# Performance work log

Measured on AMD Instinct MI355X. Metric: run time of the kernel, lower is better.

The kernel has to match this reference:

```python
import jax, jax.numpy as jnp
import numpy as np

LENGTH_SCALE = 0.1


def setup_inputs() -> dict:
    key = jax.random.key(0)
    k1, k2, k3 = jax.random.split(key, 3)
    features = jax.random.normal(k1, (8, 512, 128, 128), dtype=jnp.float32)
    # nn.Parameter init: normal(0, 0.05)
    weights = jax.random.normal(k2, (16, 64, 512), dtype=jnp.float32) * 0.05
    m = jax.random.normal(k3, (16, 64), dtype=jnp.float32)
    N = jnp.ones((64,), dtype=jnp.float32) * 12.0  # buffer init: ones * 12
    return {"features": features, "weights": weights, "m": m, "N": N}


def reference(features, weights, m, N):
    # per-class linear embedding projection: [b,f,h,w] x [e,c,f] -> [b,e,c,h,w]
    embeddings = jnp.einsum('bfhw,ecf->bechw', features, weights)
    centroids = m / N  # [e, c]
    gamma = -1.0 / (2.0 * LENGTH_SCALE ** 2)
    diff = embeddings - centroids[None, :, :, None, None]
    # squared L2, mean over embedding dim e, RBF exp -> [b, c, h, w]
    out = jnp.exp(jnp.mean(diff * diff, axis=1) * gamma)
    return out
```

## Files before the change

### kernel.cpp

```cpp
#include <hip/hip_runtime.h>

typedef __attribute__((ext_vector_type(8))) short bf16x8;
typedef __attribute__((ext_vector_type(4))) float f32x4;
typedef __attribute__((ext_vector_type(4))) float f4;
typedef __attribute__((ext_vector_type(2))) unsigned int u32x2;
typedef __attribute__((ext_vector_type(4))) unsigned int u32x4;

#define HW   16384
#define FDIM 512

__device__ __forceinline__ unsigned pkhi(float a, float b) {
    return __builtin_amdgcn_perm(__builtin_bit_cast(unsigned int, b),
                                 __builtin_bit_cast(unsigned int, a),
                                 0x07060302u);
}
__device__ __forceinline__ float trhi(float a) {
    return __builtin_bit_cast(float, __builtin_bit_cast(unsigned int, a) & 0xFFFF0000u);
}
__device__ __forceinline__ unsigned pklo(float a, float b) {
    return pkhi(a - trhi(a), b - trhi(b));
}

__global__ __launch_bounds__(256) void conv_w(const float* __restrict__ wts,
                                              unsigned short* __restrict__ wh,
                                              unsigned short* __restrict__ wl) {
    const int tid = blockIdx.x * 256 + threadIdx.x;
    const int n  = tid & 1023;
    const int kc = tid >> 10;
    const float* src = wts + (size_t)((n & 15) * 64 + (n >> 4)) * FDIM + kc * 8;
    f4 a = *(const f4*)src, b = *(const f4*)(src + 4);
    u32x4 h = { pkhi(a[0], a[1]), pkhi(a[2], a[3]), pkhi(b[0], b[1]), pkhi(b[2], b[3]) };
    u32x4 l = { pklo(a[0], a[1]), pklo(a[2], a[3]), pklo(b[0], b[1]), pklo(b[2], b[3]) };
    size_t off = ((size_t)kc * 1024 + n) * 8;
    *(u32x4*)(wh + off) = h;
    *(u32x4*)(wl + off) = l;
}

__global__ __launch_bounds__(256, 4) void duq_main(
    const float* __restrict__ feat,
    const unsigned short* __restrict__ wh,
    const unsigned short* __restrict__ wl,
    const float* __restrict__ m_in,
    const float* __restrict__ n_in,
    float* __restrict__ out)
{
    __shared__ __align__(16) unsigned short Ah[128 * 40];
    __shared__ __align__(16) unsigned short Al[128 * 40];

    const int t  = threadIdx.x;
    const int bx = blockIdx.x;
    const int kb = bx >> 3;
    const int nb = kb & 7;
    const int mb = (bx & 7) * 128 + (kb >> 3);
    const int bidx = mb >> 7;
    const int hw0  = (mb & 127) << 7;

    const int fb = t & 7;
    const int pb = t >> 3;
    const float* ap = feat + (size_t)bidx * (FDIM * HW) + (size_t)(fb * 4) * HW + (hw0 + pb * 4);
    unsigned short* awH = &Ah[(pb * 4) * 40 + fb * 4];
    unsigned short* awL = &Al[(pb * 4) * 40 + fb * 4];

    const int lane = t & 63;
    const int wv = t >> 6;
    const int wm = wv >> 1, wn = wv & 1;
    const int l16 = lane & 15, qd = lane >> 4;

    const unsigned short* arH = &Ah[(wm * 64 + l16) * 40 + qd * 8];
    const unsigned short* arL = &Al[(wm * 64 + l16) * 40 + qd * 8];

    const size_t bgoff = ((size_t)qd * 1024 + (size_t)(nb * 128 + wn * 64 + l16)) * 8;
    const unsigned short* bgh = wh + bgoff;
    const unsigned short* bgl = wl + bgoff;

    f32x4 acc[4][4] = {};

    f4 av[4];
    #pragma unroll
    for (int i = 0; i < 4; ++i) av[i] = *(const f4*)(ap + (size_t)i * HW);

    bf16x8 cbh = *(const bf16x8*)(bgh);
    bf16x8 cbl = *(const bf16x8*)(bgl);
    size_t boff = 0;

    for (int kt = 0; kt < 16; ++kt) {
        __syncthreads();
        #pragma unroll
        for (int j = 0; j < 4; ++j) {
            float a0 = av[0][j], a1 = av[1][j], a2 = av[2][j], a3 = av[3][j];
            u32x2 h, l;
            h[0] = pkhi(a0, a1); h[1] = pkhi(a2, a3);
            l[0] = pklo(a0, a1); l[1] = pklo(a2, a3);
            *(u32x2*)(awH + j * 40) = h;
            *(u32x2*)(awL + j * 40) = l;
        }
        __syncthreads();

        if (kt < 15) {
            ap += 32 * HW;
            #pragma unroll
            for (int i = 0; i < 4; ++i) av[i] = *(const f4*)(ap + (size_t)i * HW);
        }

        bf16x8 fah[4], fal[4];
        #pragma unroll
        for (int i = 0; i < 4; ++i) {
            fah[i] = *(const bf16x8*)(arH + i * 640);
            fal[i] = *(const bf16x8*)(arL + i * 640);
        }

        #pragma unroll
        for (int j = 0; j < 4; ++j) {
            size_t bnext = boff + ((j == 3) ? (size_t)(32768 - 384) : (size_t)128);
            bf16x8 nbh = *(const bf16x8*)(bgh + bnext);
            bf16x8 nbl = *(const bf16x8*)(bgl + bnext);
            #pragma unroll
            for (int i = 0; i < 4; ++i) {
                acc[i][j] = __builtin_amdgcn_mfma_f32_16x16x32_bf16(fah[i], cbh, acc[i][j], 0, 0, 0);
                acc[i][j] = __builtin_amdgcn_mfma_f32_16x16x32_bf16(fah[i], cbl, acc[i][j], 0, 0, 0);
                acc[i][j] = __builtin_amdgcn_mfma_f32_16x16x32_bf16(fal[i], cbh, acc[i][j], 0, 0, 0);
            }
            cbh = nbh; cbl = nbl; boff = bnext;
        }
    }

    float centv[4];
    #pragma unroll
    for (int j = 0; j < 4; ++j) {
        int cj = nb * 8 + wn * 4 + j;
        centv[j] = m_in[l16 * 64 + cj] / n_in[cj];
    }
    #pragma unroll
    for (int i = 0; i < 4; ++i) {
        #pragma unroll
        for (int j = 0; j < 4; ++j) {
            float s0 = acc[i][j][0] - centv[j]; s0 *= s0;
            float s1 = acc[i][j][1] - centv[j]; s1 *= s1;
            float s2 = acc[i][j][2] - centv[j]; s2 *= s2;
            float s3 = acc[i][j][3] - centv[j]; s3 *= s3;
            #pragma unroll
            for (int msk = 1; msk < 16; msk <<= 1) {
                s0 += __shfl_xor(s0, msk, 64);
                s1 += __shfl_xor(s1, msk, 64);
                s2 += __shfl_xor(s2, msk, 64);
                s3 += __shfl_xor(s3, msk, 64);
            }
            if (l16 == 0) {
                int cj = nb * 8 + wn * 4 + j;
                f4 o;
                o[0] = __expf(s0 * -3.125f);
                o[1] = __expf(s1 * -3.125f);
                o[2] = __expf(s2 * -3.125f);
                o[3] = __expf(s3 * -3.125f);
                size_t off = ((size_t)(bidx * 64 + cj)) * HW
                           + (size_t)(hw0 + wm * 64 + i * 16 + qd * 4);
                *(f4*)(out + off) = o;
            }
        }
    }
}

__global__ __launch_bounds__(256) void duq_fallback(
    const float* __restrict__ feat, const float* __restrict__ wts,
    const float* __restrict__ m_in, const float* __restrict__ n_in,
    float* __restrict__ out)
{
    __shared__ __align__(16) unsigned short Ah[128 * 40];
    __shared__ __align__(16) unsigned short Al[128 * 40];
    __shared__ __align__(16) unsigned short Bh[128 * 40];
    __shared__ __align__(16) unsigned short Bl[128 * 40];

    const int t  = threadIdx.x;
    const int bx = blockIdx.x;
    const int nb = bx & 7;
    const int mb = bx >> 3;
    const int bidx = mb >> 7;
    const int hw0  = (mb & 127) << 7;

    const int fb = t & 7;
    const int pb = t >> 3;
    const float* ap = feat + (size_t)bidx * (FDIM * HW) + (size_t)(fb * 4) * HW + (hw0 + pb * 4);

    const int bn  = t >> 1;
    const int bh_ = t & 1;
    const int ng  = nb * 128 + bn;
    const float* bp = wts + (size_t)((ng & 15) * 64 + (ng >> 4)) * FDIM + bh_ * 16;

    unsigned short* awH = &Ah[(pb * 4) * 40 + fb * 4];
    unsigned short* awL = &Al[(pb * 4) * 40 + fb * 4];
    unsigned short* bwH = &Bh[bn * 40 + bh_ * 16];
    unsigned short* bwL = &Bl[bn * 40 + bh_ * 16];

    const int lane = t & 63;
    const int wv = t >> 6;
    const int wm = wv >> 1, wn = wv & 1;
    const int l16 = lane & 15, qd = lane >> 4;

    const unsigned short* arH = &Ah[(wm * 64 + l16) * 40 + qd * 8];
    const unsigned short* arL = &Al[(wm * 64 + l16) * 40 + qd * 8];
    const unsigned short* brH = &Bh[(wn * 64 + l16) * 40 + qd * 8];
    const unsigned short* brL = &Bl[(wn * 64 + l16) * 40 + qd * 8];

    f32x4 acc[4][4] = {};

    f4 av[4], bv[4];
    #pragma unroll
    for (int i = 0; i < 4; ++i) av[i] = *(const f4*)(ap + (size_t)i * HW);
    #pragma unroll
    for (int q = 0; q < 4; ++q) bv[q] = *(const f4*)(bp + q * 4);

    for (int kt = 0; kt < 16; ++kt) {
        __syncthreads();
        #pragma unroll
        for (int j = 0; j < 4; ++j) {
            float a0 = av[0][j], a1 = av[1][j], a2 = av[2][j], a3 = av[3][j];
            u32x2 h, l;
            h[0] = pkhi(a0, a1); h[1] = pkhi(a2, a3);
            l[0] = pklo(a0, a1); l[1] = pklo(a2, a3);
            *(u32x2*)(awH + j * 40) = h;
            *(u32x2*)(awL + j * 40) = l;
        }
        {
            u32x4 h0 = { pkhi(bv[0][0], bv[0][1]), pkhi(bv[0][2], bv[0][3]),
                         pkhi(bv[1][0], bv[1][1]), pkhi(bv[1][2], bv[1][3]) };
            u32x4 h1 = { pkhi(bv[2][0], bv[2][1]), pkhi(bv[2][2], bv[2][3]),
                         pkhi(bv[3][0], bv[3][1]), pkhi(bv[3][2], bv[3][3]) };
            u32x4 l0 = { pklo(bv[0][0], bv[0][1]), pklo(bv[0][2], bv[0][3]),
                         pklo(bv[1][0], bv[1][1]), pklo(bv[1][2], bv[1][3]) };
            u32x4 l1 = { pklo(bv[2][0], bv[2][1]), pklo(bv[2][2], bv[2][3]),
                         pklo(bv[3][0], bv[3][1]), pklo(bv[3][2], bv[3][3]) };
            *(u32x4*)(bwH)     = h0;  *(u32x4*)(bwH + 8) = h1;
            *(u32x4*)(bwL)     = l0;  *(u32x4*)(bwL + 8) = l1;
        }
        __syncthreads();

        if (kt < 15) {
            ap += 32 * HW;
            bp += 32;
            #pragma unroll
            for (int i = 0; i < 4; ++i) av[i] = *(const f4*)(ap + (size_t)i * HW);
            #pragma unroll
            for (int q = 0; q < 4; ++q) bv[q] = *(const f4*)(bp + q * 4);
        }

        bf16x8 fah[4], fal[4];
        #pragma unroll
        for (int i = 0; i < 4; ++i) {
            fah[i] = *(const bf16x8*)(arH + i * 640);
            fal[i] = *(const bf16x8*)(arL + i * 640);
        }
        #pragma unroll
        for (int j = 0; j < 4; ++j) {
            bf16x8 fbh = *(const bf16x8*)(brH + j * 640);
            bf16x8 fbl = *(const bf16x8*)(brL + j * 640);
            #pragma unroll
            for (int i = 0; i < 4; ++i) {
                acc[i][j] = __builtin_amdgcn_mfma_f32_16x16x32_bf16(fah[i], fbh, acc[i][j], 0, 0, 0);
                acc[i][j] = __builtin_amdgcn_mfma_f32_16x16x32_bf16(fah[i], fbl, acc[i][j], 0, 0, 0);
                acc[i][j] = __builtin_amdgcn_mfma_f32_16x16x32_bf16(fal[i], fbh, acc[i][j], 0, 0, 0);
            }
        }
    }

    float centv[4];
    #pragma unroll
    for (int j = 0; j < 4; ++j) {
        int cj = nb * 8 + wn * 4 + j;
        centv[j] = m_in[l16 * 64 + cj] / n_in[cj];
    }
    #pragma unroll
    for (int i = 0; i < 4; ++i) {
        #pragma unroll
        for (int j = 0; j < 4; ++j) {
            float s0 = acc[i][j][0] - centv[j]; s0 *= s0;
            float s1 = acc[i][j][1] - centv[j]; s1 *= s1;
            float s2 = acc[i][j][2] - centv[j]; s2 *= s2;
            float s3 = acc[i][j][3] - centv[j]; s3 *= s3;
            #pragma unroll
            for (int msk = 1; msk < 16; msk <<= 1) {
                s0 += __shfl_xor(s0, msk, 64);
                s1 += __shfl_xor(s1, msk, 64);
                s2 += __shfl_xor(s2, msk, 64);
                s3 += __shfl_xor(s3, msk, 64);
            }
            if (l16 == 0) {
                int cj = nb * 8 + wn * 4 + j;
                f4 o;
                o[0] = __expf(s0 * -3.125f);
                o[1] = __expf(s1 * -3.125f);
                o[2] = __expf(s2 * -3.125f);
                o[3] = __expf(s3 * -3.125f);
                size_t off = ((size_t)(bidx * 64 + cj)) * HW
                           + (size_t)(hw0 + wm * 64 + i * 16 + qd * 4);
                *(f4*)(out + off) = o;
            }
        }
    }
}

extern "C" void kernel_launch(void* const* d_in, const int* in_sizes, int n_in,
                              void* d_out, int out_size, void* d_ws, size_t ws_size,
                              hipStream_t stream) {
    const float* feat = (const float*)d_in[0];
    const float* wts  = (const float*)d_in[1];
    const float* mbuf = (const float*)d_in[2];
    const float* nbuf = (const float*)d_in[3];
    float* out = (float*)d_out;

    if (ws_size >= (size_t)(2 * 1024 * 1024 + 128 * 1024)) {
        unsigned short* wh = (unsigned short*)d_ws;
        unsigned short* wl = wh + 512 * 1024;
        conv_w<<<dim3(256), dim3(256), 0, stream>>>(wts, wh, wl);
        duq_main<<<dim3(1024 * 8), dim3(256), 0, stream>>>(feat, wh, wl, mbuf, nbuf, out);
    } else {
        duq_fallback<<<dim3(1024 * 8), dim3(256), 0, stream>>>(feat, wts, mbuf, nbuf, out);
    }
}
```

Baseline: 707.8 us.

## Load A fragments directly from global into registers, dropping LDS staging

Replaces the shared-memory staging of feature tiles, with its bf16 hi/lo split and barriers, by per-wave direct global loads into registers arranged in MFMA fragment order. A register double buffer prefetches the next k-slice while the current one is computed, and launch bounds drop to two blocks per CU. This removes the LDS round trip and the block-wide syncs. The cost is scalar loads instead of vector loads, each feature element read twice across waves, and higher register use.

```diff
diff --git a/kernel.cpp b/kernel.cpp
--- a/kernel.cpp
+++ b/kernel.cpp
@@ -36,7 +36,7 @@
     *(u32x4*)(wl + off) = l;
 }
 
-__global__ __launch_bounds__(256, 4) void duq_main(
+__global__ __launch_bounds__(256, 2) void duq_direct(
     const float* __restrict__ feat,
     const unsigned short* __restrict__ wh,
     const unsigned short* __restrict__ wl,
@@ -44,9 +44,6 @@
     const float* __restrict__ n_in,
     float* __restrict__ out)
 {
-    __shared__ __align__(16) unsigned short Ah[128 * 40];
-    __shared__ __align__(16) unsigned short Al[128 * 40];
-
     const int t  = threadIdx.x;
     const int bx = blockIdx.x;
     const int kb = bx >> 3;
@@ -55,19 +52,13 @@
     const int bidx = mb >> 7;
     const int hw0  = (mb & 127) << 7;
 
-    const int fb = t & 7;
-    const int pb = t >> 3;
-    const float* ap = feat + (size_t)bidx * (FDIM * HW) + (size_t)(fb * 4) * HW + (hw0 + pb * 4);
-    unsigned short* awH = &Ah[(pb * 4) * 40 + fb * 4];
-    unsigned short* awL = &Al[(pb * 4) * 40 + fb * 4];
-
     const int lane = t & 63;
     const int wv = t >> 6;
     const int wm = wv >> 1, wn = wv & 1;
     const int l16 = lane & 15, qd = lane >> 4;
 
-    const unsigned short* arH = &Ah[(wm * 64 + l16) * 40 + qd * 8];
-    const unsigned short* arL = &Al[(wm * 64 + l16) * 40 + qd * 8];
+    const float* apc = feat + (size_t)bidx * (FDIM * HW)
+                     + (size_t)(qd * 8) * HW + (hw0 + wm * 64 + l16);
 
     const size_t bgoff = ((size_t)qd * 1024 + (size_t)(nb * 128 + wn * 64 + l16)) * 8;
     const unsigned short* bgh = wh + bgoff;
@@ -75,40 +66,31 @@
 
     f32x4 acc[4][4] = {};
 
-    f4 av[4];
-    #pragma unroll
-    for (int i = 0; i < 4; ++i) av[i] = *(const f4*)(ap + (size_t)i * HW);
-
     bf16x8 cbh = *(const bf16x8*)(bgh);
     bf16x8 cbl = *(const bf16x8*)(bgl);
     size_t boff = 0;
 
-    for (int kt = 0; kt < 16; ++kt) {
-        __syncthreads();
-        #pragma unroll
-        for (int j = 0; j < 4; ++j) {
-            float a0 = av[0][j], a1 = av[1][j], a2 = av[2][j], a3 = av[3][j];
-            u32x2 h, l;
-            h[0] = pkhi(a0, a1); h[1] = pkhi(a2, a3);
-            l[0] = pklo(a0, a1); l[1] = pklo(a2, a3);
-            *(u32x2*)(awH + j * 40) = h;
-            *(u32x2*)(awL + j * 40) = l;
-        }
-        __syncthreads();
-
-        if (kt < 15) {
-            ap += 32 * HW;
-            #pragma unroll
-            for (int i = 0; i < 4; ++i) av[i] = *(const f4*)(ap + (size_t)i * HW);
-        }
-
+    auto ldA = [&](float (&dst)[4][8]) {
+        #pragma unroll
+        for (int j = 0; j < 8; ++j) {
+            const float* r = apc + (size_t)j * HW;
+            #pragma unroll
+            for (int i = 0; i < 4; ++i) dst[i][j] = r[i * 16];
+        }
+        apc += 32 * HW;
+    };
+
+    auto step = [&](float (&av)[4][8]) {
         bf16x8 fah[4], fal[4];
         #pragma unroll
         for (int i = 0; i < 4; ++i) {
-            fah[i] = *(const bf16x8*)(arH + i * 640);
-            fal[i] = *(const bf16x8*)(arL + i * 640);
-        }
-
+            u32x4 hh = { pkhi(av[i][0], av[i][1]), pkhi(av[i][2], av[i][3]),
+                         pkhi(av[i][4], av[i][5]), pkhi(av[i][6], av[i][7]) };
+            u32x4 ll = { pklo(av[i][0], av[i][1]), pklo(av[i][2], av[i][3]),
+                         pklo(av[i][4], av[i][5]), pklo(av[i][6], av[i][7]) };
+            fah[i] = __builtin_bit_cast(bf16x8, hh);
+            fal[i] = __builtin_bit_cast(bf16x8, ll);
+        }
         #pragma unroll
         for (int j = 0; j < 4; ++j) {
             size_t bnext = boff + ((j == 3) ? (size_t)(32768 - 384) : (size_t)128);
@@ -122,6 +104,16 @@
             }
             cbh = nbh; cbl = nbl; boff = bnext;
         }
+    };
+
+    float avA[4][8], avB[4][8];
+    ldA(avA);
+    #pragma unroll 1
+    for (int kt2 = 0; kt2 < 8; ++kt2) {
+        ldA(avB);
+        step(avA);
+        if (kt2 < 7) ldA(avA);
+        step(avB);
     }
 
     float centv[4];
@@ -311,7 +303,7 @@
         unsigned short* wh = (unsigned short*)d_ws;
         unsigned short* wl = wh + 512 * 1024;
         conv_w<<<dim3(256), dim3(256), 0, stream>>>(wts, wh, wl);
-        duq_main<<<dim3(1024 * 8), dim3(256), 0, stream>>>(feat, wh, wl, mbuf, nbuf, out);
+        duq_direct<<<dim3(1024 * 8), dim3(256), 0, stream>>>(feat, wh, wl, mbuf, nbuf, out);
     } else {
         duq_fallback<<<dim3(1024 * 8), dim3(256), 0, stream>>>(feat, wts, mbuf, nbuf, out);
     }
```

Result: faster. 691.7 us (-2.3%).
